# Performance work log

Hardware: AMD Instinct MI355X
Metric: run time of the kernel (lower is better)

Reference implementation:

```python
import jax, jax.numpy as jnp
import numpy as np

K = 2          # kernel_size == stride
EPS = 0.1      # fixed epsilon added to relu(temperature)


def setup_inputs() -> dict:
    key = jax.random.key(0)
    k1, k2 = jax.random.split(key)
    # full-positive activations, as the module expects
    x = jax.random.uniform(k1, (32, 128, 112, 112), dtype=jnp.float32)
    # temperature init: ones*initial_value + Uniform(-0.5, 0.5)
    temperature = 1.0 + (jax.random.uniform(k2, (128, 56, 56), dtype=jnp.float32) - 0.5)
    return {"x": x, "temperature": temperature}


def reference(x, temperature):
    B, C, H, W = x.shape
    Ho, Wo = H // K, W // K
    # unfold(2,K,K).unfold(3,K,K) + view -> (B,C,Ho,Wo,K*K), row-major within patch
    x_unf = (x.reshape(B, C, Ho, K, Wo, K)
               .transpose(0, 1, 2, 4, 3, 5)
               .reshape(B, C, Ho, Wo, K * K))
    temps = jax.nn.relu(temperature) + EPS            # (C,Ho,Wo)
    logits = x_unf / temps[None, :, :, :, None]       # (B,C,Ho,Wo,K*K)
    # gumbel noise, tau=1
    u = jax.random.uniform(jax.random.key(42), logits.shape,
                           dtype=logits.dtype, minval=1e-20, maxval=1.0)
    g = -jnp.log(-jnp.log(u))
    soft = jax.nn.softmax(logits + g, axis=-1)
    # hard straight-through one-hot
    hard = jax.nn.one_hot(jnp.argmax(soft, axis=-1), K * K, dtype=soft.dtype)
    samples = hard + soft - jax.lax.stop_gradient(soft)
    pooled = jnp.sum(x_unf * samples, axis=-1)        # (B,C,Ho,Wo)
    return pooled
```

## Files before the change

### kernel.cpp

```cpp
#include <hip/hip_runtime.h>
#include <math.h>
#include <stdint.h>


__device__ __forceinline__ uint32_t rotl32(uint32_t x, int d) {
    return (x << d) | (x >> (32 - d));
}

__device__ __forceinline__ uint32_t tf_xor(uint32_t x0, uint32_t x1) {
    const uint32_t ks0 = 0u;
    const uint32_t ks1 = 42u;
    const uint32_t ks2 = 0x1BD11BDAu ^ ks0 ^ ks1;
    x0 += ks0; x1 += ks1;
#define TFR(r) { x0 += x1; x1 = rotl32(x1, (r)); x1 ^= x0; }
    TFR(13) TFR(15) TFR(26) TFR(6)
    x0 += ks1; x1 += ks2 + 1u;
    TFR(17) TFR(29) TFR(16) TFR(24)
    x0 += ks2; x1 += ks0 + 2u;
    TFR(13) TFR(15) TFR(26) TFR(6)
    x0 += ks0; x1 += ks1 + 3u;
    TFR(17) TFR(29) TFR(16) TFR(24)
    x0 += ks1; x1 += ks2 + 4u;
    TFR(13) TFR(15) TFR(26) TFR(6)
    x0 += ks2; x1 += ks0 + 5u;
#undef TFR
    return x0 ^ x1;
}


__device__ __forceinline__ float flog_fast(float uf) {
    uint32_t ib = __float_as_uint(uf);
    int ex = (int)(ib >> 23) - 127;
    uint32_t mant = ib & 0x7FFFFFu;
    uint32_t up = (mant > 0x3504F3u) ? 1u : 0u;
    float e = (float)(ex + (int)up);
    float m = __uint_as_float(mant | ((127u - up) << 23));
    float r = __builtin_amdgcn_rcpf(m + 1.0f);
    float s = (m - 1.0f) * r;
    float q = s * s;
    float p = 0.22222222f;
    p = __builtin_fmaf(p, q, 0.28571429f);
    p = __builtin_fmaf(p, q, 0.4f);
    p = __builtin_fmaf(p, q, 0.66666667f);
    p = __builtin_fmaf(p, q, 2.0f);
    return __builtin_fmaf(e, 0.69314718f, s * p);
}


__device__ __forceinline__ double drcp(double b) {
#if __has_builtin(__builtin_amdgcn_rcp)
    double r = __builtin_amdgcn_rcp(b);
    r = __builtin_fma(__builtin_fma(-b, r, 1.0), r, r);
    r = __builtin_fma(__builtin_fma(-b, r, 1.0), r, r);
    return r;
#else
    return 1.0 / b;
#endif
}

__device__ __forceinline__ float flog_cr(float uf) {
    uint32_t ib = __float_as_uint(uf);
    int ex = (int)(ib >> 23) - 127;
    uint32_t mant = ib & 0x7FFFFFu;
    int up = (mant > 0x3504F3u) ? 1 : 0;
    int e = ex + up;
    uint64_t dbits = ((uint64_t)mant << 29) | ((uint64_t)(1023 - up) << 52);
    double m = __longlong_as_double((long long)dbits);
    double r = drcp(m + 1.0);
    double s = (m - 1.0) * r;
    double q = s * s;
    double p = 2.0 / 15.0;
    p = __builtin_fma(p, q, 2.0 / 13.0);
    p = __builtin_fma(p, q, 2.0 / 11.0);
    p = __builtin_fma(p, q, 2.0 / 9.0);
    p = __builtin_fma(p, q, 2.0 / 7.0);
    p = __builtin_fma(p, q, 2.0 / 5.0);
    p = __builtin_fma(p, q, 2.0 / 3.0);
    p = __builtin_fma(p, q, 2.0);
    double ln = __builtin_fma((double)e, 0x1.62e42fefa39efp-1, s * p);
    return (float)ln;
}

__device__ __forceinline__ float fexp_cr(float df) {
    double d = (double)df;
    double kd = __builtin_rint(d * 0x1.71547652b82fep+0);
    double r = __builtin_fma(kd, -0x1.62e42fefa39efp-1, d);
    r = __builtin_fma(kd, -0x1.abc9e3b39803fp-56, r);
    double p = 1.0 / 39916800.0;
    p = __builtin_fma(p, r, 1.0 / 3628800.0);
    p = __builtin_fma(p, r, 1.0 / 362880.0);
    p = __builtin_fma(p, r, 1.0 / 40320.0);
    p = __builtin_fma(p, r, 1.0 / 5040.0);
    p = __builtin_fma(p, r, 1.0 / 720.0);
    p = __builtin_fma(p, r, 1.0 / 120.0);
    p = __builtin_fma(p, r, 1.0 / 24.0);
    p = __builtin_fma(p, r, 1.0 / 6.0);
    p = __builtin_fma(p, r, 0.5);
    p = __builtin_fma(p, r, 1.0);
    p = __builtin_fma(p, r, 1.0);
    long long nb = (long long)(int)kd;
    double ev = __longlong_as_double(__double_as_longlong(p) + (nb << 52));
    return (float)ev;
}

__global__ __launch_bounds__(256) void tdgs_pool_kernel(
    const float* __restrict__ x,
    const float* __restrict__ temperature,
    float* __restrict__ out,
    int total)
{
    int n = blockIdx.x * 256 + threadIdx.x;
    if (n >= total) return;

    int w  = n % 56;
    int t  = n / 56;
    int h  = t % 56;
    int t2 = t / 56;
    int c  = t2 % 128;
    int b  = t2 / 128;

    float T = fmaxf(temperature[(c * 56 + h) * 56 + w], 0.0f) + 0.1f;

    const float* xr = x + ((size_t)(b * 128 + c) * 112 + 2 * h) * 112 + 2 * w;
    float2 r0 = *(const float2*)(xr);
    float2 r1 = *(const float2*)(xr + 112);
    float pv[4] = {r0.x, r0.y, r1.x, r1.y};

    uint32_t base = (uint32_t)n * 4u;
    float uu[4];
#pragma unroll
    for (int j = 0; j < 4; ++j) {
        uint32_t bits = tf_xor(0u, base + (uint32_t)j);
        float f = __uint_as_float((bits >> 9) | 0x3f800000u) - 1.0f;
        uu[j] = fmaxf(f + 1e-20f, 1e-20f);
    }

    float rT = __builtin_amdgcn_rcpf(T);
    float z[4];
#pragma unroll
    for (int j = 0; j < 4; ++j) {
        float l1 = flog_fast(uu[j]);
        float g  = -flog_fast(-l1);
        z[j] = __builtin_fmaf(pv[j], rT, g);
    }

    float a0 = fmaxf(z[0], z[1]), b0 = fminf(z[0], z[1]);
    float a1 = fmaxf(z[2], z[3]), b1 = fminf(z[2], z[3]);
    float m1 = fmaxf(a0, a1);
    float m2 = fmaxf(fminf(a0, a1), fmaxf(b0, b1));

    int best = 0;
    float bv = z[0];
    if (z[1] > bv) { bv = z[1]; best = 1; }
    if (z[2] > bv) { bv = z[2]; best = 2; }
    if (z[3] > bv) { bv = z[3]; best = 3; }

    const float THETA = 2.44140625e-4f;
    if (__builtin_expect(m1 - m2 < THETA, 0)) {
        float zp[4];
#pragma unroll
        for (int j = 0; j < 4; ++j) {
            float t1 = flog_cr(uu[j]);
            float g  = -flog_cr(-t1);
            zp[j] = pv[j] / T + g;
        }
        float mm = fmaxf(fmaxf(zp[0], zp[1]), fmaxf(zp[2], zp[3]));
        float e0 = fexp_cr(zp[0] - mm);
        float e1 = fexp_cr(zp[1] - mm);
        float e2 = fexp_cr(zp[2] - mm);
        float e3 = fexp_cr(zp[3] - mm);
        float s = ((e0 + e1) + e2) + e3;
        float s0 = e0 / s, s1 = e1 / s, s2 = e2 / s, s3 = e3 / s;
        best = 0;
        float bvp = s0;
        if (s1 > bvp) { bvp = s1; best = 1; }
        if (s2 > bvp) { bvp = s2; best = 2; }
        if (s3 > bvp) { bvp = s3; best = 3; }
    }

    out[n] = pv[best];
}

extern "C" void kernel_launch(void* const* d_in, const int* in_sizes, int n_in,
                              void* d_out, int out_size, void* d_ws, size_t ws_size,
                              hipStream_t stream) {
    const float* x    = (const float*)d_in[0];
    const float* temp = (const float*)d_in[1];
    float* out = (float*)d_out;

    int total = out_size;
    int blocks = (total + 255) / 256;
    tdgs_pool_kernel<<<blocks, 256, 0, stream>>>(x, temp, out, total);
}
```

Before: 350.1 us.

## Use hardware log2 with series fallback and process two outputs per thread

Replaces the software polynomial log with the hardware v_log_f32 builtin. Near u=1 it uses a short Taylor series to keep accuracy. Each thread now computes two adjacent pooled outputs, using float4 loads of x, a float2 load of temperature and a float2 store. This cuts ALU work in the Gumbel noise path and widens memory accesses. The tie-break fallback is kept but moved into a helper. The cost is more registers per thread and half as many threads, with some divergence risk from the fallback.

```diff
diff --git a/kernel.cpp b/kernel.cpp
--- a/kernel.cpp
+++ b/kernel.cpp
@@ -27,23 +27,12 @@
     return x0 ^ x1;
 }
 
-
-__device__ __forceinline__ float flog_fast(float uf) {
-    uint32_t ib = __float_as_uint(uf);
-    int ex = (int)(ib >> 23) - 127;
-    uint32_t mant = ib & 0x7FFFFFu;
-    uint32_t up = (mant > 0x3504F3u) ? 1u : 0u;
-    float e = (float)(ex + (int)up);
-    float m = __uint_as_float(mant | ((127u - up) << 23));
-    float r = __builtin_amdgcn_rcpf(m + 1.0f);
-    float s = (m - 1.0f) * r;
-    float q = s * s;
-    float p = 0.22222222f;
-    p = __builtin_fmaf(p, q, 0.28571429f);
-    p = __builtin_fmaf(p, q, 0.4f);
-    p = __builtin_fmaf(p, q, 0.66666667f);
-    p = __builtin_fmaf(p, q, 2.0f);
-    return __builtin_fmaf(e, 0.69314718f, s * p);
+__device__ __forceinline__ float hwlog2(float x) {
+#if __has_builtin(__builtin_amdgcn_logf)
+    return __builtin_amdgcn_logf(x);
+#else
+    return __log2f(x);
+#endif
 }
 
 
@@ -103,82 +92,99 @@
     return (float)ev;
 }
 
+__device__ __forceinline__ float precise_pick(const float* pv, const float* uu, float T) {
+    float zp[4];
+#pragma unroll
+    for (int j = 0; j < 4; ++j) {
+        float t1 = flog_cr(uu[j]);
+        float g  = -flog_cr(-t1);
+        zp[j] = pv[j] / T + g;
+    }
+    float mm = fmaxf(fmaxf(zp[0], zp[1]), fmaxf(zp[2], zp[3]));
+    float e0 = fexp_cr(zp[0] - mm);
+    float e1 = fexp_cr(zp[1] - mm);
+    float e2 = fexp_cr(zp[2] - mm);
+    float e3 = fexp_cr(zp[3] - mm);
+    float s = ((e0 + e1) + e2) + e3;
+    float s0 = e0 / s, s1 = e1 / s, s2 = e2 / s, s3 = e3 / s;
+    float bv = s0, sel = pv[0];
+    if (s1 > bv) { bv = s1; sel = pv[1]; }
+    if (s2 > bv) { bv = s2; sel = pv[2]; }
+    if (s3 > bv) { bv = s3; sel = pv[3]; }
+    return sel;
+}
+
 __global__ __launch_bounds__(256) void tdgs_pool_kernel(
     const float* __restrict__ x,
     const float* __restrict__ temperature,
     float* __restrict__ out,
-    int total)
+    int npairs)
 {
-    int n = blockIdx.x * 256 + threadIdx.x;
-    if (n >= total) return;
-
-    int w  = n % 56;
-    int t  = n / 56;
+    int np = blockIdx.x * 256 + threadIdx.x;
+    if (np >= npairs) return;
+
+    int w2 = np % 28;
+    int t  = np / 28;
     int h  = t % 56;
     int t2 = t / 56;
-    int c  = t2 % 128;
-    int b  = t2 / 128;
-
-    float T = fmaxf(temperature[(c * 56 + h) * 56 + w], 0.0f) + 0.1f;
-
-    const float* xr = x + ((size_t)(b * 128 + c) * 112 + 2 * h) * 112 + 2 * w;
-    float2 r0 = *(const float2*)(xr);
-    float2 r1 = *(const float2*)(xr + 112);
-    float pv[4] = {r0.x, r0.y, r1.x, r1.y};
-
-    uint32_t base = (uint32_t)n * 4u;
-    float uu[4];
-#pragma unroll
-    for (int j = 0; j < 4; ++j) {
-        uint32_t bits = tf_xor(0u, base + (uint32_t)j);
+    int c  = t2 & 127;
+    int b  = t2 >> 7;
+
+    float2 tv = *(const float2*)(temperature + (c * 56 + h) * 56 + 2 * w2);
+    float Ts[2] = { fmaxf(tv.x, 0.0f) + 0.1f, fmaxf(tv.y, 0.0f) + 0.1f };
+
+    const float* xr = x + ((size_t)(b * 128 + c) * 112 + 2 * h) * 112 + 4 * w2;
+    float4 r0 = *(const float4*)(xr);
+    float4 r1 = *(const float4*)(xr + 112);
+    float pv[2][4] = { { r0.x, r0.y, r1.x, r1.y },
+                       { r0.z, r0.w, r1.z, r1.w } };
+
+    uint32_t base = (uint32_t)np * 8u;
+    float uu[2][4];
+#pragma unroll
+    for (int k = 0; k < 8; ++k) {
+        uint32_t bits = tf_xor(0u, base + (uint32_t)k);
         float f = __uint_as_float((bits >> 9) | 0x3f800000u) - 1.0f;
-        uu[j] = fmaxf(f + 1e-20f, 1e-20f);
+        uu[k >> 2][k & 3] = fmaxf(f + 1e-20f, 1e-20f);
     }
 
-    float rT = __builtin_amdgcn_rcpf(T);
-    float z[4];
-#pragma unroll
-    for (int j = 0; j < 4; ++j) {
-        float l1 = flog_fast(uu[j]);
-        float g  = -flog_fast(-l1);
-        z[j] = __builtin_fmaf(pv[j], rT, g);
+    float res[2];
+#pragma unroll
+    for (int p = 0; p < 2; ++p) {
+        float rT = __builtin_amdgcn_rcpf(Ts[p]);
+        float z[4];
+#pragma unroll
+        for (int j = 0; j < 4; ++j) {
+            float u = uu[p][j];
+            float l1h = hwlog2(u) * 0.69314718f;
+            float d = u - 1.0f;
+            float pp = __builtin_fmaf(d, -0.25f, 0.33333333f);
+            pp = __builtin_fmaf(d, pp, -0.5f);
+            pp = __builtin_fmaf(d, pp, 1.0f);
+            float l1n = d * pp;
+            float l1 = (d > -0.015625f) ? l1n : l1h;
+            float g = hwlog2(-l1) * -0.69314718f;
+            z[j] = __builtin_fmaf(pv[p][j], rT, g);
+        }
+        float a0 = fmaxf(z[0], z[1]), b0 = fminf(z[0], z[1]);
+        float a1 = fmaxf(z[2], z[3]), b1 = fminf(z[2], z[3]);
+        float m1 = fmaxf(a0, a1);
+        float m2 = fmaxf(fminf(a0, a1), fmaxf(b0, b1));
+
+        float bv = z[0], sel = pv[p][0];
+        if (z[1] > bv) { bv = z[1]; sel = pv[p][1]; }
+        if (z[2] > bv) { bv = z[2]; sel = pv[p][2]; }
+        if (z[3] > bv) { bv = z[3]; sel = pv[p][3]; }
+
+        const float THETA = 2.44140625e-4f;
+        if (__builtin_expect(m1 - m2 < THETA, 0)) {
+            sel = precise_pick(pv[p], uu[p], Ts[p]);
+        }
+        res[p] = sel;
     }
 
-    float a0 = fmaxf(z[0], z[1]), b0 = fminf(z[0], z[1]);
-    float a1 = fmaxf(z[2], z[3]), b1 = fminf(z[2], z[3]);
-    float m1 = fmaxf(a0, a1);
-    float m2 = fmaxf(fminf(a0, a1), fmaxf(b0, b1));
-
-    int best = 0;
-    float bv = z[0];
-    if (z[1] > bv) { bv = z[1]; best = 1; }
-    if (z[2] > bv) { bv = z[2]; best = 2; }
-    if (z[3] > bv) { bv = z[3]; best = 3; }
-
-    const float THETA = 2.44140625e-4f;
-    if (__builtin_expect(m1 - m2 < THETA, 0)) {
-        float zp[4];
-#pragma unroll
-        for (int j = 0; j < 4; ++j) {
-            float t1 = flog_cr(uu[j]);
-            float g  = -flog_cr(-t1);
-            zp[j] = pv[j] / T + g;
-        }
-        float mm = fmaxf(fmaxf(zp[0], zp[1]), fmaxf(zp[2], zp[3]));
-        float e0 = fexp_cr(zp[0] - mm);
-        float e1 = fexp_cr(zp[1] - mm);
-        float e2 = fexp_cr(zp[2] - mm);
-        float e3 = fexp_cr(zp[3] - mm);
-        float s = ((e0 + e1) + e2) + e3;
-        float s0 = e0 / s, s1 = e1 / s, s2 = e2 / s, s3 = e3 / s;
-        best = 0;
-        float bvp = s0;
-        if (s1 > bvp) { bvp = s1; best = 1; }
-        if (s2 > bvp) { bvp = s2; best = 2; }
-        if (s3 > bvp) { bvp = s3; best = 3; }
-    }
-
-    out[n] = pv[best];
+    float2 o; o.x = res[0]; o.y = res[1];
+    *(float2*)(out + (size_t)np * 2) = o;
 }
 
 extern "C" void kernel_launch(void* const* d_in, const int* in_sizes, int n_in,
@@ -188,7 +194,7 @@
     const float* temp = (const float*)d_in[1];
     float* out = (float*)d_out;
 
-    int total = out_size;
-    int blocks = (total + 255) / 256;
-    tdgs_pool_kernel<<<blocks, 256, 0, stream>>>(x, temp, out, total);
-}
+    int npairs = out_size / 2;
+    int blocks = (npairs + 255) / 256;
+    tdgs_pool_kernel<<<blocks, 256, 0, stream>>>(x, temp, out, npairs);
+}
```

After: 330.5 us. 1.06x faster.
